# Performance work log

Hardware: AMD Instinct MI355X
Metric: run time of the kernel (lower is better)

Reference implementation:

```python
import jax, jax.numpy as jnp
import numpy as np

B, N, E, L, H, D = 16, 128, 2048, 4, 8, 64


def setup_inputs() -> dict:
    key = jax.random.key(0)
    k1, k2, k3, k4, k5 = jax.random.split(key, 5)
    edge_feat = jax.random.normal(k1, (B, E, D), dtype=jnp.float32)
    # index E (== num edges) is the zero-feature padding slot
    path_idx = jax.random.randint(k2, (B, N, N, L), 0, E + 1).astype(jnp.int32)
    dist = jax.random.randint(k3, (B, N, N), 0, L + 1).astype(jnp.int32)
    node_counts = jax.random.randint(k4, (B,), N // 2, N + 1).astype(jnp.int32)
    emb_table = jax.random.normal(k5, (L * H, D), dtype=jnp.float32)
    return {"edge_feat": edge_feat, "path_idx": path_idx, "dist": dist,
            "node_counts": node_counts, "emb_table": emb_table}


def reference(edge_feat, path_idx, dist, node_counts, emb_table):
    b, e, d = edge_feat.shape
    n = path_idx.shape[1]
    l = path_idx.shape[-1]
    h = emb_table.shape[0] // l
    # append zero row so padding index e gathers zeros (torch: cat zeros row)
    edata = jnp.concatenate([edge_feat, jnp.zeros((b, 1, d), edge_feat.dtype)], axis=1)
    # ragged per-graph path gather, batched: (b, n, n, l, d)
    path_data = jax.vmap(lambda ef, p: ef[p])(edata, path_idx)
    # embedding_idx = arange(h*l).reshape(l, h) -> table rows reshape to (l, h, d)
    emb = emb_table.reshape(l, h, d)
    # torch: einsum('xyld,dlh->xyh') with emb permuted (d,l,h); equivalent here
    enc = jnp.einsum('bxyld,lhd->bxyh', path_data, emb)
    dist_c = jnp.clip(dist, 1, l).astype(enc.dtype)  # clamp(min=1, max=path_len)
    enc = enc / dist_c[..., None]
    ar = jnp.arange(n)
    valid = (ar[None, :, None] < node_counts[:, None, None]) & \
            (ar[None, None, :] < node_counts[:, None, None])  # (b, n, n)
    neg_inf = jnp.asarray(-jnp.inf, enc.dtype)
    return jnp.where(valid[..., None], enc, neg_inf)
```

## Files before the change

### kernel.cpp

```cpp
#include <hip/hip_runtime.h>
#include <hip/hip_bf16.h>
#include <math.h>

#define BB 16
#define NN 128
#define EE 2048
#define LL 4
#define HH 8
#define DD 64
#define LH 32

#define NEG_SENTINEL (-1.0e30f)

__global__ __launch_bounds__(256) void precompute_proj(
    const float* __restrict__ edge_feat,
    const float* __restrict__ emb,
    __hip_bfloat16* __restrict__ proj)
{
    const int lane = threadIdx.x & 63;
    const int wave = threadIdx.x >> 6;
    const int wave_global = blockIdx.x * 4 + wave;
    const int row0 = wave_global * 4;

    float emb_r[LH];
#pragma unroll
    for (int j = 0; j < LH; ++j) emb_r[j] = emb[j * DD + lane];

    const int l5 = lane & 31;
    const int jrev = ((l5 & 1) << 4) | ((l5 & 2) << 2) | (l5 & 4) |
                     ((l5 & 8) >> 2) | ((l5 & 16) >> 4);

    for (int r = 0; r < 4; ++r) {
        const int row = row0 + r;
        const float ef = edge_feat[row * DD + lane];

        float acc[LH];
#pragma unroll
        for (int j = 0; j < LH; ++j) acc[j] = ef * emb_r[j];

#pragma unroll
        for (int s = 0; s < 5; ++s) {
            const int o = 1 << s;
            const int m = 32 >> s;
            const bool hi = (lane & o) != 0;
#pragma unroll
            for (int i = 0; i < (m >> 1); ++i) {
                float a = acc[i];
                float bv = acc[i + (m >> 1)];
                float send = hi ? a : bv;
                float recv = __shfl_xor(send, o, 64);
                acc[i] = (hi ? bv : a) + recv;
            }
        }
        const float total = acc[0] + __shfl_xor(acc[0], 32, 64);

        if (lane < 32) {
            proj[row * LH + jrev] = __float2bfloat16(total);
        }
    }
}

__global__ __launch_bounds__(256) void path_gather(
    const int* __restrict__ path_idx,
    const int* __restrict__ dist,
    const int* __restrict__ node_counts,
    const __hip_bfloat16* __restrict__ proj,
    __hip_bfloat16* __restrict__ out)
{
    const int pos = blockIdx.x * blockDim.x + threadIdx.x;
    const int y   = pos & (NN - 1);
    const int x   = (pos >> 7) & (NN - 1);
    const int b   = pos >> 14;

    const int4 idx4 = ((const int4*)path_idx)[pos];
    const int  dv   = dist[pos];
    const int  nc   = node_counts[b];

    const uint4* pb = (const uint4*)(proj + (size_t)b * EE * LH);

    const int idx[4] = {idx4.x, idx4.y, idx4.z, idx4.w};
    float s[HH];
#pragma unroll
    for (int h = 0; h < HH; ++h) s[h] = 0.f;

#pragma unroll
    for (int l = 0; l < LL; ++l) {
        const int  ii    = idx[l];
        const bool live  = (ii < EE);
        uint4 v = pb[min(ii, EE - 1) * 4 + l];
        if (!live) { v.x = 0u; v.y = 0u; v.z = 0u; v.w = 0u; }
        const unsigned u[4] = {v.x, v.y, v.z, v.w};
#pragma unroll
        for (int p = 0; p < 4; ++p) {
            float flo = __uint_as_float(u[p] << 16);
            float fhi = __uint_as_float(u[p] & 0xFFFF0000u);
            s[2 * p + 0] += flo;
            s[2 * p + 1] += fhi;
        }
    }

    const int   dc = dv < 1 ? 1 : (dv > LL ? LL : dv);
    const float rd = 1.0f / (float)dc;
    const bool valid = (x < nc) && (y < nc);

    uint4 ov;
    unsigned short* po = (unsigned short*)&ov;
#pragma unroll
    for (int h = 0; h < HH; ++h) {
        const float r = valid ? s[h] * rd : NEG_SENTINEL;
        __hip_bfloat16 bh = __float2bfloat16(r);
        po[h] = *(unsigned short*)&bh;
    }
    ((uint4*)out)[pos] = ov;
}

extern "C" void kernel_launch(void* const* d_in, const int* in_sizes, int n_in,
                              void* d_out, int out_size, void* d_ws, size_t ws_size,
                              hipStream_t stream) {
    const float* edge_feat   = (const float*)d_in[0];
    const int*   path_idx    = (const int*)d_in[1];
    const int*   dist        = (const int*)d_in[2];
    const int*   node_counts = (const int*)d_in[3];
    const float* emb_table   = (const float*)d_in[4];
    __hip_bfloat16* out = (__hip_bfloat16*)d_out;

    __hip_bfloat16* proj = (__hip_bfloat16*)d_ws;

    precompute_proj<<<2048, 256, 0, stream>>>(edge_feat, emb_table, proj);

    path_gather<<<1024, 256, 0, stream>>>(path_idx, dist, node_counts, proj, out);
}
```

Measured before the change: 88.52 us.

## Compute edge projection with bf16 MFMA instead of shuffle reductions

```diff
diff --git a/kernel.cpp b/kernel.cpp
--- a/kernel.cpp
+++ b/kernel.cpp
@@ -12,51 +12,69 @@
 
 #define NEG_SENTINEL (-1.0e30f)
 
-__global__ __launch_bounds__(256) void precompute_proj(
+typedef __attribute__((ext_vector_type(8))) short bf16x8;
+typedef __attribute__((ext_vector_type(4))) float f32x4;
+
+__device__ inline short f2bf(float f) {
+    __hip_bfloat16 h = __float2bfloat16(f);
+    return *(short*)&h;
+}
+
+__device__ inline bf16x8 pack_bf8(float4 a, float4 b) {
+    bf16x8 r;
+    r[0] = f2bf(a.x); r[1] = f2bf(a.y); r[2] = f2bf(a.z); r[3] = f2bf(a.w);
+    r[4] = f2bf(b.x); r[5] = f2bf(b.y); r[6] = f2bf(b.z); r[7] = f2bf(b.w);
+    return r;
+}
+
+__global__ __launch_bounds__(256) void precompute_proj_mfma(
     const float* __restrict__ edge_feat,
     const float* __restrict__ emb,
     __hip_bfloat16* __restrict__ proj)
 {
     const int lane = threadIdx.x & 63;
     const int wave = threadIdx.x >> 6;
-    const int wave_global = blockIdx.x * 4 + wave;
-    const int row0 = wave_global * 4;
+    const int tile = blockIdx.x * 4 + wave;
+    const int row0 = tile * 16;
+    const int m    = lane & 15;
+    const int quad = lane >> 4;
 
-    float emb_r[LH];
-#pragma unroll
-    for (int j = 0; j < LH; ++j) emb_r[j] = emb[j * DD + lane];
+    const float* arow = edge_feat + (size_t)(row0 + m) * DD + quad * 8;
+    const float4 a00 = ((const float4*)arow)[0];
+    const float4 a01 = ((const float4*)arow)[1];
+    const float4 a10 = ((const float4*)(arow + 32))[0];
+    const float4 a11 = ((const float4*)(arow + 32))[1];
 
-    const int l5 = lane & 31;
-    const int jrev = ((l5 & 1) << 4) | ((l5 & 2) << 2) | (l5 & 4) |
-                     ((l5 & 8) >> 2) | ((l5 & 16) >> 4);
+    const float* br0 = emb + (size_t)m * DD + quad * 8;
+    const float* br1 = emb + (size_t)(16 + m) * DD + quad * 8;
+    const float4 b000 = ((const float4*)br0)[0];
+    const float4 b001 = ((const float4*)br0)[1];
+    const float4 b010 = ((const float4*)(br0 + 32))[0];
+    const float4 b011 = ((const float4*)(br0 + 32))[1];
+    const float4 b100 = ((const float4*)br1)[0];
+    const float4 b101 = ((const float4*)br1)[1];
+    const float4 b110 = ((const float4*)(br1 + 32))[0];
+    const float4 b111 = ((const float4*)(br1 + 32))[1];
 
-    for (int r = 0; r < 4; ++r) {
-        const int row = row0 + r;
-        const float ef = edge_feat[row * DD + lane];
+    const bf16x8 aK0  = pack_bf8(a00, a01);
+    const bf16x8 aK1  = pack_bf8(a10, a11);
+    const bf16x8 b0K0 = pack_bf8(b000, b001);
+    const bf16x8 b0K1 = pack_bf8(b010, b011);
+    const bf16x8 b1K0 = pack_bf8(b100, b101);
+    const bf16x8 b1K1 = pack_bf8(b110, b111);
 
-        float acc[LH];
-#pragma unroll
-        for (int j = 0; j < LH; ++j) acc[j] = ef * emb_r[j];
+    f32x4 acc0 = {0.f, 0.f, 0.f, 0.f};
+    f32x4 acc1 = {0.f, 0.f, 0.f, 0.f};
+    acc0 = __builtin_amdgcn_mfma_f32_16x16x32_bf16(aK0, b0K0, acc0, 0, 0, 0);
+    acc0 = __builtin_amdgcn_mfma_f32_16x16x32_bf16(aK1, b0K1, acc0, 0, 0, 0);
+    acc1 = __builtin_amdgcn_mfma_f32_16x16x32_bf16(aK0, b1K0, acc1, 0, 0, 0);
+    acc1 = __builtin_amdgcn_mfma_f32_16x16x32_bf16(aK1, b1K1, acc1, 0, 0, 0);
 
 #pragma unroll
-        for (int s = 0; s < 5; ++s) {
-            const int o = 1 << s;
-            const int m = 32 >> s;
-            const bool hi = (lane & o) != 0;
-#pragma unroll
-            for (int i = 0; i < (m >> 1); ++i) {
-                float a = acc[i];
-                float bv = acc[i + (m >> 1)];
-                float send = hi ? a : bv;
-                float recv = __shfl_xor(send, o, 64);
-                acc[i] = (hi ? bv : a) + recv;
-            }
-        }
-        const float total = acc[0] + __shfl_xor(acc[0], 32, 64);
-
-        if (lane < 32) {
-            proj[row * LH + jrev] = __float2bfloat16(total);
-        }
+    for (int r = 0; r < 4; ++r) {
+        const int row = row0 + quad * 4 + r;
+        proj[row * LH + m]      = __float2bfloat16(acc0[r]);
+        proj[row * LH + 16 + m] = __float2bfloat16(acc1[r]);
     }
 }
 
@@ -126,7 +144,7 @@
 
     __hip_bfloat16* proj = (__hip_bfloat16*)d_ws;
 
-    precompute_proj<<<2048, 256, 0, stream>>>(edge_feat, emb_table, proj);
+    precompute_proj_mfma<<<512, 256, 0, stream>>>(edge_feat, emb_table, proj);
 
     path_gather<<<1024, 256, 0, stream>>>(path_idx, dist, node_counts, proj, out);
 }
```

New measurement: 78.75 us. 11.0% less time.
